# Kernel optimization log

Measured on AMD Instinct MI355X. Metric: run time of the kernel, lower is better.

Reference implementation:

```python
import jax, jax.numpy as jnp
import numpy as np

N, E, IN, HID, HEADS, OUT = 50000, 800000, 184, 64, 4, 2
LRELU_SLOPE = 0.2
LN_EPS = 1e-5


def setup_inputs() -> dict:
    key = jax.random.key(0)
    ks = jax.random.split(key, 20)
    p = lambda k, s: jax.random.normal(k, s, jnp.float32) * 0.05
    return {
        'x': jax.random.normal(ks[0], (N, IN), jnp.float32),
        'edge_index': jax.random.randint(ks[1], (2, E), 0, N, jnp.int64),
        'Wp': p(ks[2], (IN, HID)), 'bp': p(ks[3], (HID,)),
        'W0': p(ks[4], (HID, HEADS * HID)), 'as0': p(ks[5], (HEADS, HID)), 'ad0': p(ks[6], (HEADS, HID)), 'b0': p(ks[7], (HEADS * HID,)),
        'W1': p(ks[8], (HEADS * HID, HEADS * HID)), 'as1': p(ks[9], (HEADS, HID)), 'ad1': p(ks[10], (HEADS, HID)), 'b1': p(ks[11], (HEADS * HID,)),
        'W2': p(ks[12], (HEADS * HID, OUT)), 'as2': p(ks[13], (1, OUT)), 'ad2': p(ks[14], (1, OUT)), 'b2': p(ks[15], (OUT,)),
        'ln_g': jnp.ones((HEADS * HID,), jnp.float32), 'ln_b': jnp.zeros((HEADS * HID,), jnp.float32),
    }


def _layernorm(x, g, b):
    mu = jnp.mean(x, axis=-1, keepdims=True)
    var = jnp.mean(jnp.square(x - mu), axis=-1, keepdims=True)
    return (x - mu) * jax.lax.rsqrt(var + LN_EPS) * g + b


def _gat_conv(x, src, dst, n, W, a_s, a_d, b, heads, c):
    # x: [n, in]; PyG GATConv: per-head linear, edge attention, segment softmax over dst, scatter-add
    h = (x @ W).reshape(n, heads, c)                 # [n, H, C]
    al_s = jnp.sum(h * a_s, axis=-1)                  # [n, H]
    al_d = jnp.sum(h * a_d, axis=-1)                  # [n, H]
    e = jax.nn.leaky_relu(al_s[src] + al_d[dst], LRELU_SLOPE)   # [E, H]
    m = jax.ops.segment_max(e, dst, num_segments=n)   # per-dst max (self-loops ensure nonempty)
    ex = jnp.exp(e - m[dst])
    den = jax.ops.segment_sum(ex, dst, num_segments=n)
    alpha = ex / (den[dst] + 1e-16)                   # PyG softmax eps
    msg = h[src] * alpha[:, :, None]                  # [E, H, C]
    out = jax.ops.segment_sum(msg, dst, num_segments=n)
    return out.reshape(n, heads * c) + b


def reference(x, edge_index, Wp, bp, W0, as0, ad0, b0, W1, as1, ad1, b1, W2, as2, ad2, b2, ln_g, ln_b):
    n = x.shape[0]
    loop = jnp.arange(n, dtype=edge_index.dtype)      # add_self_loops=True
    src = jnp.concatenate([edge_index[0], loop])
    dst = jnp.concatenate([edge_index[1], loop])

    h = x @ Wp + bp                                   # input_proj -> [n, HID]
    # layer 0: out dim HID*HEADS==256 -> norm; residual skipped (x_res is [n, HID])
    h = _gat_conv(h, src, dst, n, W0, as0, ad0, b0, HEADS, HID)
    h = jax.nn.elu(_layernorm(h, ln_g, ln_b))
    # dropout: eval mode (identity)
    # layer 1: norm + residual + elu
    h_res = h
    h = _gat_conv(h, src, dst, n, W1, as1, ad1, b1, HEADS, HID)
    h = jax.nn.elu(_layernorm(h, ln_g, ln_b) + h_res)
    # layer 2 (last): heads=1, no norm/activation
    return _gat_conv(h, src, dst, n, W2, as2, ad2, b2, 1, OUT)
```

## Files before the change

kernel.cpp:

```cpp
#include <hip/hip_runtime.h>
#include <hip/hip_bf16.h>
#include <cmath>
#include <cfloat>

constexpr int IN_DIM = 184;
constexpr int KP     = 192;
constexpr int HID    = 64;
constexpr int HEADS  = 4;
constexpr int F1     = HEADS * HID;
constexpr float SLOPE = 0.2f;
constexpr float LN_EPS = 1e-5f;

using short8 = __attribute__((ext_vector_type(8))) short;
using f32x4  = __attribute__((ext_vector_type(4))) float;

__device__ inline float b2f(ushort u) {
    return __uint_as_float(((unsigned)u) << 16);
}
__device__ inline ushort f2b(float f) {
    __hip_bfloat16 b = __float2bfloat16(f);
    return *reinterpret_cast<ushort*>(&b);
}
__device__ inline float lrelu(float e) { return e > 0.f ? e : SLOPE * e; }
__device__ inline float fexp(float x) { return __expf(x); }
__device__ inline float frcp(float x) { return __builtin_amdgcn_rcpf(x); }

__device__ inline size_t frag_idx(int k, int c) {
    int kt = k >> 5, kk = k & 31;
    int q = (kk & 15) >> 2, j = (kk & 3) | ((kk >> 4) << 2);
    int w = c >> 6, ct = (c >> 4) & 3, lr = c & 15;
    int lane = (q << 4) | lr;
    return ((((size_t)kt * 4 + w) * 4 + ct) * 64 + lane) * 8 + j;
}

__device__ inline void edge_sd(const int* __restrict__ ei, int E, int idx, int& s, int& d) {
    if (idx < E) { s = ei[idx]; d = ei[E + idx]; }
    else         { s = idx - E; d = idx - E; }
}

__global__ __launch_bounds__(256) void weight_prep(const float* __restrict__ Wp,
                                                   const float* __restrict__ W0,
                                                   const float* __restrict__ bp,
                                                   const float* __restrict__ W1,
                                                   ushort* __restrict__ Wf0,
                                                   float* __restrict__ bc,
                                                   ushort* __restrict__ Wf1,
                                                   const int* __restrict__ ei,
                                                   int E, int Etot,
                                                   int* __restrict__ deg) {
    int b = blockIdx.x, c = threadIdx.x;
    if (b < KP) {
        int k = b;
        float s = 0.f;
        if (k < IN_DIM)
            for (int j = 0; j < HID; ++j) s = fmaf(Wp[k * HID + j], W0[j * F1 + c], s);
        Wf0[frag_idx(k, c)] = f2b(s);
        if (k == 0) {
            float bs = 0.f;
            for (int j = 0; j < HID; ++j) bs = fmaf(bp[j], W0[j * F1 + c], bs);
            bc[c] = bs;
        }
    } else if (b < KP + F1) {
        int k = b - KP;
        Wf1[frag_idx(k, c)] = f2b(W1[(size_t)k * F1 + c]);
    } else {
        int idx = (b - KP - F1) * 256 + c;
        if (idx < Etot) {
            int s, d; edge_sd(ei, E, idx, s, d);
            atomicAdd(&deg[d], 1);
        }
    }
}

template<int KSTEPS, bool L0>
__global__ __launch_bounds__(256) void mfma_gemm2(const void* __restrict__ Xv,
                                                  const ushort* __restrict__ Wfrag,
                                                  const float* __restrict__ bc,
                                                  const float* __restrict__ as_,
                                                  const float* __restrict__ ad_,
                                                  unsigned char* __restrict__ F8,
                                                  float* __restrict__ rscale,
                                                  float* __restrict__ als,
                                                  float* __restrict__ ald,
                                                  int M,
                                                  int gemm_blocks,
                                                  const int* __restrict__ ei,
                                                  int E, int Etot,
                                                  int* __restrict__ wcur,
                                                  int* __restrict__ csr_src) {
    const int tid = threadIdx.x;

    if (L0 && (int)blockIdx.x >= gemm_blocks) {
        int base = (blockIdx.x - gemm_blocks) * 512 + tid;
#pragma unroll
        for (int r = 0; r < 2; ++r) {
            int idx = base + r * 256;
            if (idx < Etot) {
                int s, d; edge_sd(ei, E, idx, s, d);
                int pos = atomicAdd(&wcur[d], 1);
                csr_src[pos] = s;
            }
        }
        return;
    }

    const int w = tid >> 6, l = tid & 63;
    const int lr = l & 15, q = l >> 4;
    const int row0 = blockIdx.x * 64;

    __shared__ ushort a_lds[2][64][40];
    __shared__ float rmax_lds[64][4];

    const int srow = tid >> 2, seg = tid & 3;
    int grow = row0 + srow; if (grow >= M) grow = M - 1;

    auto stage = [&](int buf, int kt) {
        if constexpr (!L0) {
            const ushort* p = (const ushort*)Xv + (size_t)grow * 256 + kt * 32 + seg * 8;
            *(uint4*)&a_lds[buf][srow][seg * 8] = *(const uint4*)p;
        } else {
            int kb = kt * 32 + seg * 8;
            uint4 o = {0u, 0u, 0u, 0u};
            if (kb < IN_DIM) {
                const float* p = (const float*)Xv + (size_t)grow * IN_DIM + kb;
                float4 lo = *(const float4*)p;
                float4 hi = *(const float4*)(p + 4);
                o.x = (uint)f2b(lo.x) | ((uint)f2b(lo.y) << 16);
                o.y = (uint)f2b(lo.z) | ((uint)f2b(lo.w) << 16);
                o.z = (uint)f2b(hi.x) | ((uint)f2b(hi.y) << 16);
                o.w = (uint)f2b(hi.z) | ((uint)f2b(hi.w) << 16);
            }
            *(uint4*)&a_lds[buf][srow][seg * 8] = o;
        }
    };

    f32x4 acc[4][4] = {};

    stage(0, 0);
    short8 bcur[4];
#pragma unroll
    for (int ct = 0; ct < 4; ++ct) {
        const ushort* bp = Wfrag + ((((size_t)0 * 4 + w) * 4 + ct) * 64 + l) * 8;
        short8 b; *(uint4*)&b = *(const uint4*)bp; bcur[ct] = b;
    }
    __syncthreads();

    int buf = 0;
#pragma unroll
    for (int kt = 0; kt < KSTEPS; ++kt) {
        short8 bnext[4];
        if (kt + 1 < KSTEPS) {
#pragma unroll
            for (int ct = 0; ct < 4; ++ct) {
                const ushort* bp = Wfrag + ((((size_t)(kt + 1) * 4 + w) * 4 + ct) * 64 + l) * 8;
                short8 b; *(uint4*)&b = *(const uint4*)bp; bnext[ct] = b;
            }
            stage(buf ^ 1, kt + 1);
        }
        short8 afr[4];
#pragma unroll
        for (int rt = 0; rt < 4; ++rt) {
            short8 a;
            *(uint2*)&a       = *(const uint2*)&a_lds[buf][rt * 16 + lr][4 * q];
            *((uint2*)&a + 1) = *(const uint2*)&a_lds[buf][rt * 16 + lr][4 * q + 16];
            afr[rt] = a;
        }
#pragma unroll
        for (int rt = 0; rt < 4; ++rt)
#pragma unroll
            for (int ct = 0; ct < 4; ++ct)
                acc[rt][ct] = __builtin_amdgcn_mfma_f32_16x16x32_bf16(afr[rt], bcur[ct], acc[rt][ct], 0, 0, 0);
        __syncthreads();
        if (kt + 1 < KSTEPS) {
#pragma unroll
            for (int ct = 0; ct < 4; ++ct) bcur[ct] = bnext[ct];
        }
        buf ^= 1;
    }

    if constexpr (L0) {
        float bcv[4];
#pragma unroll
        for (int ct = 0; ct < 4; ++ct) bcv[ct] = bc[w * 64 + ct * 16 + lr];
#pragma unroll
        for (int rt = 0; rt < 4; ++rt)
#pragma unroll
            for (int ct = 0; ct < 4; ++ct)
#pragma unroll
                for (int r = 0; r < 4; ++r) acc[rt][ct][r] += bcv[ct];
    }

#pragma unroll
    for (int rt = 0; rt < 4; ++rt) {
#pragma unroll
        for (int r = 0; r < 4; ++r) {
            float m = fmaxf(fmaxf(fabsf(acc[rt][0][r]), fabsf(acc[rt][1][r])),
                            fmaxf(fabsf(acc[rt][2][r]), fabsf(acc[rt][3][r])));
            m = fmaxf(m, __shfl_xor(m, 1));
            m = fmaxf(m, __shfl_xor(m, 2));
            m = fmaxf(m, __shfl_xor(m, 4));
            m = fmaxf(m, __shfl_xor(m, 8));
            if (lr == 0) rmax_lds[rt * 16 + q * 4 + r][w] = m;
        }
    }
    __syncthreads();

#pragma unroll
    for (int rt = 0; rt < 4; ++rt) {
#pragma unroll
        for (int r = 0; r < 4; ++r) {
            int lrow = rt * 16 + q * 4 + r;
            float m = fmaxf(fmaxf(rmax_lds[lrow][0], rmax_lds[lrow][1]),
                            fmaxf(rmax_lds[lrow][2], rmax_lds[lrow][3]));
            float inv = (m > 0.f) ? 127.f / m : 0.f;
            int row = row0 + lrow;
            if (row < M) {
#pragma unroll
                for (int ct = 0; ct < 4; ++ct) {
                    int qv = (int)rintf(acc[rt][ct][r] * inv) + 128;
                    qv = min(max(qv, 0), 255);
                    F8[(size_t)row * 256 + w * 64 + ct * 16 + lr] = (unsigned char)qv;
                }
                if (w == 0 && lr == 0) rscale[row] = m * (1.f / 127.f);
            }
        }
    }

    float asv[4], adv[4];
#pragma unroll
    for (int ct = 0; ct < 4; ++ct) {
        asv[ct] = as_[w * 64 + ct * 16 + lr];
        adv[ct] = ad_[w * 64 + ct * 16 + lr];
    }
#pragma unroll
    for (int rt = 0; rt < 4; ++rt) {
#pragma unroll
        for (int r = 0; r < 4; ++r) {
            float ls = 0.f, ld_ = 0.f;
#pragma unroll
            for (int ct = 0; ct < 4; ++ct) {
                ls  = fmaf(acc[rt][ct][r], asv[ct], ls);
                ld_ = fmaf(acc[rt][ct][r], adv[ct], ld_);
            }
            for (int off = 8; off; off >>= 1) {
                ls  += __shfl_xor(ls, off);
                ld_ += __shfl_xor(ld_, off);
            }
            int row = row0 + rt * 16 + q * 4 + r;
            if (lr == 0 && row < M) {
                als[row * HEADS + w] = ls;
                ald[row * HEADS + w] = ld_;
            }
        }
    }
}

__global__ __launch_bounds__(256) void scan1(const int* __restrict__ deg, int* __restrict__ out,
                                             int* __restrict__ csum, int N) {
    __shared__ int s[256];
    int t = threadIdx.x;
    int idx0 = blockIdx.x * 1024 + t * 4;
    int v[4];
#pragma unroll
    for (int i = 0; i < 4; ++i) { int id = idx0 + i; v[i] = (id < N) ? deg[id] : 0; }
    int sum = v[0] + v[1] + v[2] + v[3];
    s[t] = sum; __syncthreads();
    for (int off = 1; off < 256; off <<= 1) {
        int x = (t >= off) ? s[t - off] : 0;
        __syncthreads();
        s[t] += x;
        __syncthreads();
    }
    int run = (t == 0) ? 0 : s[t - 1];
#pragma unroll
    for (int i = 0; i < 4; ++i) {
        run += v[i];
        int id = idx0 + i;
        if (id < N) out[id] = run;
    }
    if (t == 255) csum[blockIdx.x] = s[255];
}

__global__ __launch_bounds__(256) void scan2(int* __restrict__ csum, int M) {
    __shared__ int s[256];
    int t = threadIdx.x;
    s[t] = (t < M) ? csum[t] : 0;
    __syncthreads();
    for (int off = 1; off < 256; off <<= 1) {
        int x = (t >= off) ? s[t - off] : 0;
        __syncthreads();
        s[t] += x;
        __syncthreads();
    }
    if (t < M) csum[t] = s[t];
}

__global__ __launch_bounds__(256) void scan3(const int* __restrict__ deg, int* __restrict__ rend,
                                             const int* __restrict__ csum, int* __restrict__ wcur, int N) {
    int id = blockIdx.x * 256 + threadIdx.x;
    if (id >= N) return;
    int chunk = id >> 10;
    int off = (chunk == 0) ? 0 : csum[chunk - 1];
    int e = rend[id] + off;
    rend[id] = e;
    wcur[id] = e - deg[id];
}

template<bool RES, bool FEAT2>
__global__ __launch_bounds__(128) void aggregate_fused(const int* __restrict__ csr_src,
                                                       const int* __restrict__ rend,
                                                       const int* __restrict__ deg_,
                                                       const unsigned char* __restrict__ feat,
                                                       const float* __restrict__ rscale,
                                                       const float* __restrict__ als,
                                                       const float* __restrict__ ald,
                                                       const float* __restrict__ bias,
                                                       const float* __restrict__ g,
                                                       const float* __restrict__ bln,
                                                       const ushort* __restrict__ res,
                                                       ushort* __restrict__ out_bf,
                                                       const float* __restrict__ W2,
                                                       const float* __restrict__ as2,
                                                       const float* __restrict__ ad2,
                                                       float4* __restrict__ nf2,
                                                       int N) {
    __shared__ __align__(16) float alds[2][64][4];
    __shared__ int srcs[2][64];
    const int w = threadIdx.x >> 6, l = threadIdx.x & 63;
    const int n = blockIdx.x * 2 + w;
    if (n >= N) return;
    const int dg = deg_[n], end = rend[n], start = end - dg;
    const int hf = l >> 5;
    const int lh = l & 31;
    const int hh = lh >> 3;
    const float4 ad4 = ((const float4*)ald)[n];

    float acc[8] = {0.f, 0.f, 0.f, 0.f, 0.f, 0.f, 0.f, 0.f};
    float accC = 0.f;

    auto fma8 = [&](uint2 u, float b) {
        acc[0] = fmaf((float)( u.x        & 0xffu), b, acc[0]);
        acc[1] = fmaf((float)((u.x >>  8) & 0xffu), b, acc[1]);
        acc[2] = fmaf((float)((u.x >> 16) & 0xffu), b, acc[2]);
        acc[3] = fmaf((float)( u.x >> 24         ), b, acc[3]);
        acc[4] = fmaf((float)( u.y        & 0xffu), b, acc[4]);
        acc[5] = fmaf((float)((u.y >>  8) & 0xffu), b, acc[5]);
        acc[6] = fmaf((float)((u.y >> 16) & 0xffu), b, acc[6]);
        acc[7] = fmaf((float)( u.y >> 24         ), b, acc[7]);
        accC += b;
    };

    auto LD = [&](int j) -> uint2 {
        int s = srcs[w][j];
        return *(const uint2*)&feat[(size_t)s * 256 + lh * 8];
    };

    auto gather_chunk = [&](int cnt) {
        int j = hf;
        for (; j + 2 < cnt; j += 4) {
            uint2 u0 = LD(j);
            uint2 u1 = LD(j + 2);
            fma8(u0, alds[w][j][hh]);
            fma8(u1, alds[w][j + 2][hh]);
        }
        for (; j < cnt; j += 2) {
            uint2 u0 = LD(j);
            fma8(u0, alds[w][j][hh]);
        }
    };

    if (dg <= 64) {
        int s = 0;
        float sc = 0.f;
        float4 ex = { 0.f, 0.f, 0.f, 0.f };
        if (l < dg) {
            s = csr_src[start + l];
            float4 a = ((const float4*)als)[s];
            sc = rscale[s];
            ex.x = fexp(lrelu(a.x + ad4.x));
            ex.y = fexp(lrelu(a.y + ad4.y));
            ex.z = fexp(lrelu(a.z + ad4.z));
            ex.w = fexp(lrelu(a.w + ad4.w));
        }
        float4 sum = ex;
        for (int off = 32; off; off >>= 1) {
            sum.x += __shfl_xor(sum.x, off);
            sum.y += __shfl_xor(sum.y, off);
            sum.z += __shfl_xor(sum.z, off);
            sum.w += __shfl_xor(sum.w, off);
        }
        float4 al = { ex.x * frcp(sum.x + 1e-16f) * sc, ex.y * frcp(sum.y + 1e-16f) * sc,
                      ex.z * frcp(sum.z + 1e-16f) * sc, ex.w * frcp(sum.w + 1e-16f) * sc };
        *(float4*)&alds[w][l][0] = al;
        srcs[w][l] = s;
        __builtin_amdgcn_s_waitcnt(0);
        gather_chunk(dg);
    } else {
        float4 sum = { 0.f, 0.f, 0.f, 0.f };
        for (int i = l; i < dg; i += 64) {
            int s = csr_src[start + i];
            float4 a = ((const float4*)als)[s];
            sum.x += fexp(lrelu(a.x + ad4.x));
            sum.y += fexp(lrelu(a.y + ad4.y));
            sum.z += fexp(lrelu(a.z + ad4.z));
            sum.w += fexp(lrelu(a.w + ad4.w));
        }
        for (int off = 32; off; off >>= 1) {
            sum.x += __shfl_xor(sum.x, off);
            sum.y += __shfl_xor(sum.y, off);
            sum.z += __shfl_xor(sum.z, off);
            sum.w += __shfl_xor(sum.w, off);
        }
        float4 inv = { frcp(sum.x + 1e-16f), frcp(sum.y + 1e-16f),
                       frcp(sum.z + 1e-16f), frcp(sum.w + 1e-16f) };
        for (int c0 = start; c0 < end; c0 += 64) {
            int cnt = min(64, end - c0);
            if (l < cnt) {
                int s = csr_src[c0 + l];
                float4 a = ((const float4*)als)[s];
                float sc = rscale[s];
                float4 al = { fexp(lrelu(a.x + ad4.x)) * inv.x * sc,
                              fexp(lrelu(a.y + ad4.y)) * inv.y * sc,
                              fexp(lrelu(a.z + ad4.z)) * inv.z * sc,
                              fexp(lrelu(a.w + ad4.w)) * inv.w * sc };
                *(float4*)&alds[w][l][0] = al;
                srcs[w][l] = s;
            }
            __builtin_amdgcn_s_waitcnt(0);
            gather_chunk(cnt);
        }
    }

#pragma unroll
    for (int r = 0; r < 8; ++r) acc[r] += __shfl_xor(acc[r], 32);
    accC += __shfl_xor(accC, 32);

    float4 bv0 = ((const float4*)bias)[lh * 2];
    float4 bv1 = ((const float4*)bias)[lh * 2 + 1];
    float c128 = 128.f * accC;
    float v[8] = { acc[0] - c128 + bv0.x, acc[1] - c128 + bv0.y,
                   acc[2] - c128 + bv0.z, acc[3] - c128 + bv0.w,
                   acc[4] - c128 + bv1.x, acc[5] - c128 + bv1.y,
                   acc[6] - c128 + bv1.z, acc[7] - c128 + bv1.w };
    float sm = v[0] + v[1] + v[2] + v[3] + v[4] + v[5] + v[6] + v[7];
    for (int off = 32; off; off >>= 1) sm += __shfl_xor(sm, off);
    float mu = sm * (1.f / (2 * F1));
    float dv = 0.f;
#pragma unroll
    for (int r = 0; r < 8; ++r) { float d = v[r] - mu; dv += d * d; }
    for (int off = 32; off; off >>= 1) dv += __shfl_xor(dv, off);
    float rstd = rsqrtf(dv * (1.f / (2 * F1)) + LN_EPS);
    float4 gv0 = ((const float4*)g)[lh * 2],   gv1 = ((const float4*)g)[lh * 2 + 1];
    float4 lb0 = ((const float4*)bln)[lh * 2], lb1 = ((const float4*)bln)[lh * 2 + 1];
    float y[8];
    y[0] = (v[0] - mu) * rstd * gv0.x + lb0.x;
    y[1] = (v[1] - mu) * rstd * gv0.y + lb0.y;
    y[2] = (v[2] - mu) * rstd * gv0.z + lb0.z;
    y[3] = (v[3] - mu) * rstd * gv0.w + lb0.w;
    y[4] = (v[4] - mu) * rstd * gv1.x + lb1.x;
    y[5] = (v[5] - mu) * rstd * gv1.y + lb1.y;
    y[6] = (v[6] - mu) * rstd * gv1.z + lb1.z;
    y[7] = (v[7] - mu) * rstd * gv1.w + lb1.w;
    if (RES) {
        uint4 rr = ((const uint4*)res)[(size_t)n * 32 + lh];
        y[0] += __uint_as_float(rr.x << 16);
        y[1] += __uint_as_float(rr.x & 0xffff0000u);
        y[2] += __uint_as_float(rr.y << 16);
        y[3] += __uint_as_float(rr.y & 0xffff0000u);
        y[4] += __uint_as_float(rr.z << 16);
        y[5] += __uint_as_float(rr.z & 0xffff0000u);
        y[6] += __uint_as_float(rr.w << 16);
        y[7] += __uint_as_float(rr.w & 0xffff0000u);
    }
#pragma unroll
    for (int r = 0; r < 8; ++r) y[r] = y[r] > 0.f ? y[r] : fexp(y[r]) - 1.f;

    if (!FEAT2) {
        if (l < 32) {
            uint4 o;
            o.x = (uint)f2b(y[0]) | ((uint)f2b(y[1]) << 16);
            o.y = (uint)f2b(y[2]) | ((uint)f2b(y[3]) << 16);
            o.z = (uint)f2b(y[4]) | ((uint)f2b(y[5]) << 16);
            o.w = (uint)f2b(y[6]) | ((uint)f2b(y[7]) << 16);
            ((uint4*)out_bf)[(size_t)n * 32 + lh] = o;
        }
    } else {
        const float4* W24 = (const float4*)W2;
        float c0 = 0.f, c1 = 0.f;
#pragma unroll
        for (int j = 0; j < 4; ++j) {
            float4 wv = W24[lh * 4 + j];
            c0 += y[2 * j] * wv.x + y[2 * j + 1] * wv.z;
            c1 += y[2 * j] * wv.y + y[2 * j + 1] * wv.w;
        }
        for (int off = 32; off; off >>= 1) {
            c0 += __shfl_xor(c0, off);
            c1 += __shfl_xor(c1, off);
        }
        c0 *= 0.5f; c1 *= 0.5f;
        if (l == 0) {
            float4 o = { c0, c1,
                         c0 * as2[0] + c1 * as2[1],
                         c0 * ad2[0] + c1 * ad2[1] };
            nf2[n] = o;
        }
    }
}

__global__ __launch_bounds__(128) void layer2_fused(const int* __restrict__ csr_src,
                                                    const int* __restrict__ rend,
                                                    const int* __restrict__ deg_,
                                                    const float4* __restrict__ nf2,
                                                    const float* __restrict__ b2,
                                                    float* __restrict__ out, int N) {
    const int w = threadIdx.x >> 6, l = threadIdx.x & 63;
    const int n = blockIdx.x * 2 + w;
    if (n >= N) return;
    const int dg = deg_[n], end = rend[n], start = end - dg;
    const float ad = nf2[n].w;

    float a0 = 0.f, a1 = 0.f;
    if (dg <= 64) {
        float ex = 0.f;
        float f0 = 0.f, f1 = 0.f;
        if (l < dg) {
            int s = csr_src[start + l];
            float4 v = nf2[s];
            ex = fexp(lrelu(v.z + ad));
            f0 = v.x; f1 = v.y;
        }
        float sum = ex;
        for (int off = 32; off; off >>= 1) sum += __shfl_xor(sum, off);
        float al = ex * frcp(sum + 1e-16f);
        a0 = f0 * al; a1 = f1 * al;
    } else {
        float sum = 0.f;
        for (int i = l; i < dg; i += 64) {
            int s = csr_src[start + i];
            sum += fexp(lrelu(nf2[s].z + ad));
        }
        for (int off = 32; off; off >>= 1) sum += __shfl_xor(sum, off);
        float inv = frcp(sum + 1e-16f);
        for (int i = l; i < dg; i += 64) {
            int s = csr_src[start + i];
            float4 v = nf2[s];
            float al = fexp(lrelu(v.z + ad)) * inv;
            a0 = fmaf(v.x, al, a0);
            a1 = fmaf(v.y, al, a1);
        }
    }
    for (int off = 32; off; off >>= 1) {
        a0 += __shfl_xor(a0, off);
        a1 += __shfl_xor(a1, off);
    }
    if (l == 0) {
        out[(size_t)n * 2 + 0] = a0 + b2[0];
        out[(size_t)n * 2 + 1] = a1 + b2[1];
    }
}

extern "C" void kernel_launch(void* const* d_in, const int* in_sizes, int n_in,
                              void* d_out, int out_size, void* d_ws, size_t ws_size,
                              hipStream_t stream) {
    const float* x    = (const float*)d_in[0];
    const int*   ei   = (const int*)d_in[1];
    const float* Wp   = (const float*)d_in[2];
    const float* bp   = (const float*)d_in[3];
    const float* W0   = (const float*)d_in[4];
    const float* as0  = (const float*)d_in[5];
    const float* ad0  = (const float*)d_in[6];
    const float* b0   = (const float*)d_in[7];
    const float* W1   = (const float*)d_in[8];
    const float* as1  = (const float*)d_in[9];
    const float* ad1  = (const float*)d_in[10];
    const float* b1   = (const float*)d_in[11];
    const float* W2   = (const float*)d_in[12];
    const float* as2  = (const float*)d_in[13];
    const float* ad2  = (const float*)d_in[14];
    const float* b2   = (const float*)d_in[15];
    const float* ln_g = (const float*)d_in[16];
    const float* ln_b = (const float*)d_in[17];
    float* out = (float*)d_out;

    const int N    = in_sizes[0] / IN_DIM;
    const int E    = in_sizes[1] / 2;
    const int Etot = E + N;

    char* wptr = (char*)d_ws;
    auto alloc = [&](size_t bytes) -> void* {
        void* p = wptr;
        wptr += (bytes + 255) & ~(size_t)255;
        return p;
    };
    unsigned char* F8 = (unsigned char*)alloc((size_t)N * F1);
    float*  rscale = (float*)alloc(sizeof(float) * (size_t)N);
    ushort* Ab     = (ushort*)alloc(sizeof(ushort) * (size_t)N * F1);
    float*  als    = (float*)alloc(sizeof(float) * (size_t)N * HEADS);
    float*  ald    = (float*)alloc(sizeof(float) * (size_t)N * HEADS);
    float4* nf2    = (float4*)alloc(sizeof(float4) * (size_t)N);
    ushort* Wf0    = (ushort*)alloc(sizeof(ushort) * (size_t)F1 * KP);
    float*  bc     = (float*)alloc(sizeof(float) * F1);
    ushort* Wf1    = (ushort*)alloc(sizeof(ushort) * (size_t)F1 * F1);
    int*    deg    = (int*)alloc(sizeof(int) * (size_t)N);
    int*    rend   = (int*)alloc(sizeof(int) * (size_t)N);
    int*    wcur   = (int*)alloc(sizeof(int) * (size_t)N);
    int*    csum   = (int*)alloc(sizeof(int) * 256);
    int*    csrs   = (int*)alloc(sizeof(int) * (size_t)Etot);

    const int eb   = (Etot + 255) / 256;
    const int eb2  = (Etot + 511) / 512;
    const int nb   = (N + 255) / 256;
    const int nb2  = (N + 1) / 2;
    const int nchunks = (N + 1023) / 1024;
    const int mb64 = (N + 63) / 64;

    hipMemsetAsync(deg, 0, sizeof(int) * (size_t)N, stream);
    weight_prep<<<KP + F1 + eb, 256, 0, stream>>>(Wp, W0, bp, W1, Wf0, bc, Wf1,
                                                  ei, E, Etot, deg);

    scan1<<<nchunks, 256, 0, stream>>>(deg, rend, csum, N);
    scan2<<<1, 256, 0, stream>>>(csum, nchunks);
    scan3<<<nb, 256, 0, stream>>>(deg, rend, csum, wcur, N);

    mfma_gemm2<KP / 32, true><<<mb64 + eb2, 256, 0, stream>>>(
        x, Wf0, bc, as0, ad0, F8, rscale, als, ald, N,
        mb64, ei, E, Etot, wcur, csrs);
    aggregate_fused<false, false><<<nb2, 128, 0, stream>>>(csrs, rend, deg, F8, rscale,
        als, ald, b0, ln_g, ln_b, nullptr, Ab, nullptr, nullptr, nullptr, nullptr, N);

    mfma_gemm2<F1 / 32, false><<<mb64, 256, 0, stream>>>(
        Ab, Wf1, nullptr, as1, ad1, F8, rscale, als, ald, N,
        mb64, nullptr, 0, 0, nullptr, nullptr);
    aggregate_fused<true, true><<<nb2, 128, 0, stream>>>(csrs, rend, deg, F8, rscale,
        als, ald, b1, ln_g, ln_b, Ab, nullptr, W2, as2, ad2, nf2, N);

    layer2_fused<<<nb2, 128, 0, stream>>>(csrs, rend, deg, nf2, b2, out, N);
}
```

Measured before the change: 262.7 us.

## Interleave GEMM and CSR-fill blocks and fold scan2 into scan3

The fused layer-0 GEMM/CSR-fill kernel now interleaves its two block types: every third block index is a GEMM tile, and the rest are edge-scatter blocks whose index is recomputed from the block id. Before, all GEMM blocks came first and all fill blocks after. The mix is meant to run compute-heavy MFMA tiles alongside atomic-heavy scatter work on the CUs. Separately, the single-block scan2 launch is removed, and scan3 instead sums the preceding chunk totals serially in each thread. This saves one kernel launch and its dependency, at the cost of up to about 49 redundant cached loads per thread.

```diff
diff --git a/kernel.cpp b/kernel.cpp
--- a/kernel.cpp
+++ b/kernel.cpp
@@ -89,24 +89,37 @@
                                                   int* __restrict__ wcur,
                                                   int* __restrict__ csr_src) {
     const int tid = threadIdx.x;
-
-    if (L0 && (int)blockIdx.x >= gemm_blocks) {
-        int base = (blockIdx.x - gemm_blocks) * 512 + tid;
-#pragma unroll
-        for (int r = 0; r < 2; ++r) {
-            int idx = base + r * 256;
-            if (idx < Etot) {
-                int s, d; edge_sd(ei, E, idx, s, d);
-                int pos = atomicAdd(&wcur[d], 1);
-                csr_src[pos] = s;
-            }
-        }
-        return;
+    int tile;
+
+    if constexpr (L0) {
+        const int bid = blockIdx.x;
+        const int gq = bid / 3, gr = bid - gq * 3;
+        const bool is_gemm = (gr == 0) && (gq < gemm_blocks);
+        if (!is_gemm) {
+            int fid = bid - min(gq + (gr ? 1 : 0) + (gr == 0 ? 1 : 0) - (gr == 0 ? 1 : 0), 0);
+            int ng = min(gq + (gr > 0 ? 1 : 0), gemm_blocks);
+            if (gr == 0 && gq >= gemm_blocks) ng = gemm_blocks;
+            fid = bid - ng - (gr == 0 && gq < gemm_blocks ? 1 : 0);
+            int base = fid * 512 + tid;
+#pragma unroll
+            for (int r = 0; r < 2; ++r) {
+                int idx = base + r * 256;
+                if (idx < Etot) {
+                    int s, d; edge_sd(ei, E, idx, s, d);
+                    int pos = atomicAdd(&wcur[d], 1);
+                    csr_src[pos] = s;
+                }
+            }
+            return;
+        }
+        tile = gq;
+    } else {
+        tile = blockIdx.x;
     }
 
     const int w = tid >> 6, l = tid & 63;
     const int lr = l & 15, q = l >> 4;
-    const int row0 = blockIdx.x * 64;
+    const int row0 = tile * 64;
 
     __shared__ ushort a_lds[2][64][40];
     __shared__ float rmax_lds[64][4];
@@ -281,26 +294,13 @@
     if (t == 255) csum[blockIdx.x] = s[255];
 }
 
-__global__ __launch_bounds__(256) void scan2(int* __restrict__ csum, int M) {
-    __shared__ int s[256];
-    int t = threadIdx.x;
-    s[t] = (t < M) ? csum[t] : 0;
-    __syncthreads();
-    for (int off = 1; off < 256; off <<= 1) {
-        int x = (t >= off) ? s[t - off] : 0;
-        __syncthreads();
-        s[t] += x;
-        __syncthreads();
-    }
-    if (t < M) csum[t] = s[t];
-}
-
 __global__ __launch_bounds__(256) void scan3(const int* __restrict__ deg, int* __restrict__ rend,
                                              const int* __restrict__ csum, int* __restrict__ wcur, int N) {
     int id = blockIdx.x * 256 + threadIdx.x;
     if (id >= N) return;
     int chunk = id >> 10;
-    int off = (chunk == 0) ? 0 : csum[chunk - 1];
+    int off = 0;
+    for (int i = 0; i < chunk; ++i) off += csum[i];
     int e = rend[id] + off;
     rend[id] = e;
     wcur[id] = e - deg[id];
@@ -619,12 +619,14 @@
                                                   ei, E, Etot, deg);
 
     scan1<<<nchunks, 256, 0, stream>>>(deg, rend, csum, N);
-    scan2<<<1, 256, 0, stream>>>(csum, nchunks);
     scan3<<<nb, 256, 0, stream>>>(deg, rend, csum, wcur, N);
 
-    mfma_gemm2<KP / 32, true><<<mb64 + eb2, 256, 0, stream>>>(
-        x, Wf0, bc, as0, ad0, F8, rscale, als, ald, N,
-        mb64, ei, E, Etot, wcur, csrs);
+    {
+        int total = mb64 + eb2;
+        mfma_gemm2<KP / 32, true><<<total, 256, 0, stream>>>(
+            x, Wf0, bc, as0, ad0, F8, rscale, als, ald, N,
+            mb64, ei, E, Etot, wcur, csrs);
+    }
     aggregate_fused<false, false><<<nb2, 128, 0, stream>>>(csrs, rend, deg, F8, rscale,
         als, ald, b0, ln_g, ln_b, nullptr, Ab, nullptr, nullptr, nullptr, nullptr, N);
 
```

Result: faster. 250.7 us (-4.5%).
